# Optimization experiments

Hardware: AMD Instinct MI355X
Metric: run time of the kernel (lower is better)

The kernel has to match this reference:

```python
import jax, jax.numpy as jnp
import numpy as np

B = 4096
INPUT_DIM = 4096
N_BLOCKS = 8
BLOCK = INPUT_DIM // N_BLOCKS  # 512
N_EXPERTS = 6
H = 1024   # expert_hidden
H2 = H // 2


def setup_inputs() -> dict:
    key = jax.random.key(0)
    ks = jax.random.split(key, 16)
    s = 0.02  # init scale keeps tanh/softmax in sane range
    return {
        "x":   jax.random.normal(ks[0], (B, INPUT_DIM), jnp.float32),
        # routers: per-block stacked weights [8, ...]
        "Wr1": jax.random.normal(ks[1], (N_BLOCKS, BLOCK, 32), jnp.float32) * s,
        "br1": jax.random.normal(ks[2], (N_BLOCKS, 32), jnp.float32) * s,
        "Wr2": jax.random.normal(ks[3], (N_BLOCKS, 32, N_EXPERTS), jnp.float32) * s,
        "br2": jax.random.normal(ks[4], (N_BLOCKS, N_EXPERTS), jnp.float32) * s,
        # experts: stacked [6, ...], shared across all 8 blocks
        "We1": jax.random.normal(ks[5], (N_EXPERTS, BLOCK, H), jnp.float32) * s,
        "be1": jax.random.normal(ks[6], (N_EXPERTS, H), jnp.float32) * s,
        "We2": jax.random.normal(ks[7], (N_EXPERTS, H, H2), jnp.float32) * s,
        "be2": jax.random.normal(ks[8], (N_EXPERTS, H2), jnp.float32) * s,
        "We3": jax.random.normal(ks[9], (N_EXPERTS, H2, 3), jnp.float32) * s,
        "be3": jax.random.normal(ks[10], (N_EXPERTS, 3), jnp.float32) * s,
        # aggregator
        "Wa1": jax.random.normal(ks[11], (3, 16), jnp.float32) * s,
        "ba1": jax.random.normal(ks[12], (16,), jnp.float32) * s,
        "Wa2": jax.random.normal(ks[13], (16, 3), jnp.float32) * s,
        "ba2": jax.random.normal(ks[14], (3,), jnp.float32) * s,
    }


def reference(x, Wr1, br1, Wr2, br2, We1, be1, We2, be2, We3, be3,
              Wa1, ba1, Wa2, ba2):
    b = x.shape[0]
    blocks = x.reshape(b, N_BLOCKS, BLOCK)                       # [b,s,d]
    # routers (one per block s)
    r1 = jax.nn.relu(jnp.einsum('bsd,sdh->bsh', blocks, Wr1) + br1)
    routing = jax.nn.softmax(
        jnp.einsum('bsh,she->bse', r1, Wr2) + br2, axis=-1)      # [b,s,E]
    # experts applied to every block (grouped GEMMs)
    h1 = jnp.tanh(jnp.einsum('bsd,edh->bseh', blocks, We1) + be1)        # [b,s,E,H]
    h2 = jnp.tanh(jnp.einsum('bseh,ehk->bsek', h1, We2) + be2)           # [b,s,E,H2]
    eo = jnp.einsum('bsek,eko->bseo', h2, We3) + be3                     # [b,s,E,3]
    weighted = jnp.einsum('bse,bseo->bso', routing, eo)                  # [b,s,3]
    final = weighted.mean(axis=1)                                        # mean over 8 blocks
    a1 = jax.nn.relu(final @ Wa1 + ba1)
    return a1 @ Wa2 + ba2                                                # [b,3]
```

## Files before the change

kernel.cpp:

```cpp
#include <hip/hip_runtime.h>
#include <cstdint>
#include <cstddef>

typedef __bf16 bf16;
typedef __bf16 bf16x4 __attribute__((ext_vector_type(4)));
typedef __bf16 bf16x8 __attribute__((ext_vector_type(8)));
typedef float  f32x4  __attribute__((ext_vector_type(4)));
typedef long long i64v;

#define NROWS   32768
#define DBLK    512
#define H1N     1024
#define H2N     512
#define NEXP    6
#define NBATCH  4096
#define HALL    (NEXP * H1N)
#define W2SCALE 32.0f
#define W2INV   0.03125f

__device__ __forceinline__ void gld16(const void* g, void* l) {
    __builtin_amdgcn_global_load_lds(
        (const __attribute__((address_space(1))) void*)g,
        (__attribute__((address_space(3))) void*)l, 16, 0, 0);
}

__device__ __forceinline__ float fast_tanh(float x) {
    float e = __expf(2.0f * x);
    return 1.0f - __fdividef(2.0f, e + 1.0f);
}

__device__ __forceinline__ float hsum16(float v) {
    v += __shfl_xor(v, 1);
    v += __shfl_xor(v, 2);
    v += __shfl_xor(v, 4);
    v += __shfl_xor(v, 8);
    return v;
}

__device__ __forceinline__ int swz(int row, int g) {
    return row * 64 + ((g ^ (row & 7)) * 8);
}
__device__ __forceinline__ int swz8(int row, int g) {
    return row * 64 + ((g ^ ((row >> 1) & 3)) << 4);
}


__global__ void cvt_bf16_kernel(const float* __restrict__ in,
                                bf16* __restrict__ out, int n4) {
    int i = blockIdx.x * blockDim.x + threadIdx.x;
    if (i >= n4) return;
    float4 v = ((const float4*)in)[i];
    bf16x4 o;
    o.x = (bf16)v.x; o.y = (bf16)v.y; o.z = (bf16)v.z; o.w = (bf16)v.w;
    ((bf16x4*)out)[i] = o;
}

__global__ __launch_bounds__(256) void transpose_cvt(
    const float* __restrict__ in, bf16* __restrict__ out, int K, int N) {
    __shared__ bf16 tile[64][66];
    int e  = blockIdx.z;
    int n0 = blockIdx.x * 64;
    int k0 = blockIdx.y * 64;
    int c  = threadIdx.x & 63;
    int rb = threadIdx.x >> 6;
    const float* src = in + (size_t)e * K * N;
    bf16* dst = out + (size_t)e * N * K;
#pragma unroll
    for (int it = 0; it < 16; ++it) {
        int k = k0 + rb + it * 4;
        int n = n0 + c;
        if (k < K && n < N) tile[rb + it * 4][c] = (bf16)src[(size_t)k * N + n];
    }
    __syncthreads();
#pragma unroll
    for (int it = 0; it < 16; ++it) {
        int n = n0 + rb + it * 4;
        int k = k0 + c;
        if (n < N && k < K) dst[(size_t)n * K + k] = tile[c][rb + it * 4];
    }
}

__global__ __launch_bounds__(256) void transpose_cvt_fp8(
    const float* __restrict__ in, uint8_t* __restrict__ out, int K, int N,
    float scale) {
    __shared__ float tile[64][65];
    int e  = blockIdx.z;
    int n0 = blockIdx.x * 64;
    int k0 = blockIdx.y * 64;
    int c  = threadIdx.x & 63;
    int rb = threadIdx.x >> 6;
    const float* src = in + (size_t)e * K * N;
    uint8_t* dst = out + (size_t)e * N * K;
#pragma unroll
    for (int it = 0; it < 16; ++it) {
        int k = k0 + rb + it * 4;
        int n = n0 + c;
        if (k < K && n < N) tile[rb + it * 4][c] = src[(size_t)k * N + n];
    }
    __syncthreads();
#pragma unroll
    for (int it = 0; it < 16; ++it) {
        int n = n0 + rb + it * 4;
        int k = k0 + c;
        if (n < N && k < K) {
            float v = tile[c][rb + it * 4] * scale;
            int p = __builtin_amdgcn_cvt_pk_fp8_f32(v, v, 0, false);
            dst[(size_t)n * K + k] = (uint8_t)(p & 0xff);
        }
    }
}

__global__ void zero_f32_kernel(float* __restrict__ p, int n) {
    int i = blockIdx.x * blockDim.x + threadIdx.x;
    if (i < n) p[i] = 0.0f;
}


__global__ __launch_bounds__(256, 2) void router_kernel(
    const bf16* __restrict__ xbf,
    const bf16* __restrict__ Wr1t,
    const float* __restrict__ br1,
    const float* __restrict__ Wr2,
    const float* __restrict__ br2,
    float* __restrict__ routing) {
    __shared__ __align__(16) bf16 sA[128 * 64];
    __shared__ __align__(16) bf16 sB[32 * 64];
    const int tid = threadIdx.x;
    const int w = tid >> 6, l = tid & 63;
    const int s  = blockIdx.y;
    const int b0 = blockIdx.x * 128;
    const int wm = w * 32;
    const int srow = l >> 3, schk = (l & 7) * 8;
    const int fr = l & 15, fq = l >> 4;
    const bf16* Ab = xbf + (size_t)s * 512;
    const bf16* Bb = Wr1t + (size_t)s * (32 * 512);

    f32x4 acc[2][2];
#pragma unroll
    for (int i = 0; i < 2; ++i)
#pragma unroll
        for (int j = 0; j < 2; ++j) acc[i][j] = (f32x4){0.f, 0.f, 0.f, 0.f};

    for (int k0 = 0; k0 < 512; k0 += 64) {
        __syncthreads();
#pragma unroll
        for (int jj = 0; jj < 4; ++jj) {
            int row = w * 32 + jj * 8;
            gld16(Ab + (size_t)(b0 + row + srow) * 4096 + k0 + schk, sA + row * 64);
        }
        gld16(Bb + (size_t)(w * 8 + srow) * 512 + k0 + schk, sB + w * 8 * 64);
        __syncthreads();
#pragma unroll
        for (int ks = 0; ks < 2; ++ks) {
            bf16x8 af[2], bfr[2];
#pragma unroll
            for (int i = 0; i < 2; ++i)
                af[i] = *(const bf16x8*)&sA[(wm + i * 16 + fr) * 64 + ks * 32 + fq * 8];
#pragma unroll
            for (int j = 0; j < 2; ++j)
                bfr[j] = *(const bf16x8*)&sB[(j * 16 + fr) * 64 + ks * 32 + fq * 8];
#pragma unroll
            for (int i = 0; i < 2; ++i)
#pragma unroll
                for (int j = 0; j < 2; ++j)
                    acc[i][j] = __builtin_amdgcn_mfma_f32_16x16x32_bf16(
                        af[i], bfr[j], acc[i][j], 0, 0, 0);
        }
    }

    float b1v[2], w2v[2][6], br2v[6];
#pragma unroll
    for (int j = 0; j < 2; ++j) {
        int col = j * 16 + fr;
        b1v[j] = br1[s * 32 + col];
#pragma unroll
        for (int e2 = 0; e2 < 6; ++e2) w2v[j][e2] = Wr2[(s * 32 + col) * 6 + e2];
    }
#pragma unroll
    for (int e2 = 0; e2 < 6; ++e2) br2v[e2] = br2[s * 6 + e2];

#pragma unroll
    for (int i = 0; i < 2; ++i) {
#pragma unroll
        for (int r = 0; r < 4; ++r) {
            float lg[6] = {0.f, 0.f, 0.f, 0.f, 0.f, 0.f};
#pragma unroll
            for (int j = 0; j < 2; ++j) {
                float t = fmaxf(acc[i][j][r] + b1v[j], 0.f);
#pragma unroll
                for (int e2 = 0; e2 < 6; ++e2) lg[e2] += t * w2v[j][e2];
            }
#pragma unroll
            for (int e2 = 0; e2 < 6; ++e2) lg[e2] = hsum16(lg[e2]) + br2v[e2];
            float mx = lg[0];
#pragma unroll
            for (int e2 = 1; e2 < 6; ++e2) mx = fmaxf(mx, lg[e2]);
            float p[6], sum = 0.f;
#pragma unroll
            for (int e2 = 0; e2 < 6; ++e2) { p[e2] = __expf(lg[e2] - mx); sum += p[e2]; }
            float inv = __fdividef(1.f, sum);
            if (fr == 0) {
                int brow = b0 + wm + i * 16 + fq * 4 + r;
                float* dst = routing + ((size_t)brow * 8 + s) * 6;
#pragma unroll
                for (int e2 = 0; e2 < 6; ++e2) dst[e2] = p[e2] * inv;
            }
        }
    }
}

__global__ __launch_bounds__(256, 4) void gemm1_kernel(
    const bf16* __restrict__ A,
    const bf16* __restrict__ B,
    const float* __restrict__ bias,
    uint8_t* __restrict__ h1,
    int ldh) {
    __shared__ __align__(16) bf16 sA[128 * 64];
    __shared__ __align__(16) bf16 sB[128 * 64];
    const int tid = threadIdx.x;
    const int w = tid >> 6, l = tid & 63;
    const int n0 = blockIdx.x * 128;
    const int m0 = blockIdx.y * 128;
    const int wm = (w & 1) * 64, wn = (w >> 1) * 64;
    const int srow = l >> 3;
    const int gcol = ((l & 7) ^ srow) * 8;
    const int fr = l & 15, fq = l >> 4;

    f32x4 acc[4][4];
#pragma unroll
    for (int i = 0; i < 4; ++i)
#pragma unroll
        for (int j = 0; j < 4; ++j) acc[i][j] = (f32x4){0.f, 0.f, 0.f, 0.f};

    for (int k0 = 0; k0 < DBLK; k0 += 64) {
        __syncthreads();
#pragma unroll
        for (int jj = 0; jj < 4; ++jj) {
            int row = w * 32 + jj * 8;
            gld16(A + (size_t)(m0 + row + srow) * DBLK + k0 + gcol, sA + row * 64);
            gld16(B + (size_t)(n0 + row + srow) * DBLK + k0 + gcol, sB + row * 64);
        }
        __syncthreads();
#pragma unroll
        for (int ks = 0; ks < 2; ++ks) {
            bf16x8 af[4], bfr[4];
#pragma unroll
            for (int i = 0; i < 4; ++i)
                af[i] = *(const bf16x8*)&sA[swz(wm + i * 16 + fr, ks * 4 + fq)];
#pragma unroll
            for (int j = 0; j < 4; ++j)
                bfr[j] = *(const bf16x8*)&sB[swz(wn + j * 16 + fr, ks * 4 + fq)];
#pragma unroll
            for (int i = 0; i < 4; ++i)
#pragma unroll
                for (int j = 0; j < 4; ++j)
                    acc[i][j] = __builtin_amdgcn_mfma_f32_16x16x32_bf16(
                        af[i], bfr[j], acc[i][j], 0, 0, 0);
        }
    }

#pragma unroll
    for (int i = 0; i < 4; ++i) {
        int colb = m0 + wm + i * 16 + fq * 4;
        float4 bb = *(const float4*)&bias[colb];
#pragma unroll
        for (int j = 0; j < 4; ++j) {
            int xrow = n0 + wn + j * 16 + fr;
            float t0 = fast_tanh(acc[i][j][0] + bb.x);
            float t1 = fast_tanh(acc[i][j][1] + bb.y);
            float t2 = fast_tanh(acc[i][j][2] + bb.z);
            float t3 = fast_tanh(acc[i][j][3] + bb.w);
            int p = 0;
            p = __builtin_amdgcn_cvt_pk_fp8_f32(t0, t1, p, false);
            p = __builtin_amdgcn_cvt_pk_fp8_f32(t2, t3, p, true);
            *(uint32_t*)&h1[(size_t)xrow * ldh + colb] = (uint32_t)p;
        }
    }
}

__global__ __launch_bounds__(256, 4) void gemm2_kernel(
    const uint8_t* __restrict__ h1,
    const uint8_t* __restrict__ W2f8t,
    const float* __restrict__ be2,
    const float* __restrict__ We3,
    float* __restrict__ eo,
    int ldh) {
    __shared__ __align__(16) uint8_t sA[128 * 64];
    __shared__ __align__(16) uint8_t sB[128 * 64];
    __shared__ float w3s[128 * 3];
    __shared__ float b2s[128];
    const int tid = threadIdx.x;
    const int w = tid >> 6, l = tid & 63;
    const int e  = blockIdx.z;
    const int n0 = blockIdx.x * 128;
    const int m0 = blockIdx.y * 128;
    const int wm = (w & 1) * 64, wn = (w >> 1) * 64;
    const int srow4 = l >> 2;
    const int g4 = (((l & 3) ^ ((l >> 3) & 3)) << 4);
    const int fr = l & 15, fq = l >> 4;
    const uint8_t* Ae = W2f8t + (size_t)e * (H2N * H1N);
    const uint8_t* Be = h1 + (size_t)e * H1N;

    if (tid < 128) {
        int c = m0 + tid;
        b2s[tid] = be2[e * H2N + c];
        w3s[tid * 3 + 0] = We3[((size_t)e * H2N + c) * 3 + 0];
        w3s[tid * 3 + 1] = We3[((size_t)e * H2N + c) * 3 + 1];
        w3s[tid * 3 + 2] = We3[((size_t)e * H2N + c) * 3 + 2];
    }

    f32x4 acc[4][4];
#pragma unroll
    for (int i = 0; i < 4; ++i)
#pragma unroll
        for (int j = 0; j < 4; ++j) acc[i][j] = (f32x4){0.f, 0.f, 0.f, 0.f};

    for (int k0 = 0; k0 < H1N; k0 += 64) {
        __syncthreads();
#pragma unroll
        for (int jj = 0; jj < 2; ++jj) {
            int row = w * 32 + jj * 16 + srow4;
            gld16(Ae + (size_t)(m0 + row) * H1N + k0 + g4, sA + (w * 32 + jj * 16) * 64);
            gld16(Be + (size_t)(n0 + row) * ldh + k0 + g4, sB + (w * 32 + jj * 16) * 64);
        }
        __syncthreads();
#pragma unroll
        for (int ks = 0; ks < 2; ++ks) {
            i64v af[4], bfr[4];
#pragma unroll
            for (int i = 0; i < 4; ++i) {
                int row = wm + i * 16 + fr;
                af[i] = *(const i64v*)&sA[swz8(row, ks * 2 + (fq >> 1)) + ((fq & 1) << 3)];
            }
#pragma unroll
            for (int j = 0; j < 4; ++j) {
                int row = wn + j * 16 + fr;
                bfr[j] = *(const i64v*)&sB[swz8(row, ks * 2 + (fq >> 1)) + ((fq & 1) << 3)];
            }
#pragma unroll
            for (int i = 0; i < 4; ++i)
#pragma unroll
                for (int j = 0; j < 4; ++j)
                    acc[i][j] = __builtin_amdgcn_mfma_f32_16x16x32_fp8_fp8(
                        af[i], bfr[j], acc[i][j], 0, 0, 0);
        }
    }

    float p[4][3];
#pragma unroll
    for (int j = 0; j < 4; ++j) { p[j][0] = 0.f; p[j][1] = 0.f; p[j][2] = 0.f; }
#pragma unroll
    for (int i = 0; i < 4; ++i) {
        int cl = wm + i * 16 + fq * 4;
        float4 bb = *(const float4*)&b2s[cl];
        float4 wa = *(const float4*)&w3s[cl * 3 + 0];
        float4 wb = *(const float4*)&w3s[cl * 3 + 4];
        float4 wc = *(const float4*)&w3s[cl * 3 + 8];
        float bias4[4] = {bb.x, bb.y, bb.z, bb.w};
        float w30[4] = {wa.x, wa.w, wb.z, wc.y};
        float w31[4] = {wa.y, wb.x, wb.w, wc.z};
        float w32[4] = {wa.z, wb.y, wc.x, wc.w};
#pragma unroll
        for (int j = 0; j < 4; ++j) {
#pragma unroll
            for (int r = 0; r < 4; ++r) {
                float t = fast_tanh(acc[i][j][r] * W2INV + bias4[r]);
                p[j][0] += t * w30[r];
                p[j][1] += t * w31[r];
                p[j][2] += t * w32[r];
            }
        }
    }
#pragma unroll
    for (int j = 0; j < 4; ++j) {
        float v0 = p[j][0], v1 = p[j][1], v2 = p[j][2];
        v0 += __shfl_xor(v0, 16); v0 += __shfl_xor(v0, 32);
        v1 += __shfl_xor(v1, 16); v1 += __shfl_xor(v1, 32);
        v2 += __shfl_xor(v2, 16); v2 += __shfl_xor(v2, 32);
        if (fq == 0) {
            int xrow = n0 + wn + j * 16 + fr;
            float* dst = eo + ((size_t)e * NROWS + xrow) * 3;
            atomicAdd(dst + 0, v0);
            atomicAdd(dst + 1, v1);
            atomicAdd(dst + 2, v2);
        }
    }
}

__global__ void final_kernel(
    const float* __restrict__ routing, const float* __restrict__ eo,
    const float* __restrict__ be3, const float* __restrict__ Wa1,
    const float* __restrict__ ba1, const float* __restrict__ Wa2,
    const float* __restrict__ ba2, float* __restrict__ out) {
    int b = blockIdx.x * blockDim.x + threadIdx.x;
    if (b >= NBATCH) return;
    float f0 = 0.f, f1 = 0.f, f2 = 0.f;
    for (int s = 0; s < 8; ++s) {
        int r = b * 8 + s;
        const float* rt = routing + (size_t)r * 6;
#pragma unroll
        for (int e = 0; e < 6; ++e) {
            float wgt = rt[e];
            const float* eop = eo + ((size_t)e * NROWS + r) * 3;
            f0 += wgt * (eop[0] + be3[e * 3 + 0]);
            f1 += wgt * (eop[1] + be3[e * 3 + 1]);
            f2 += wgt * (eop[2] + be3[e * 3 + 2]);
        }
    }
    f0 *= 0.125f; f1 *= 0.125f; f2 *= 0.125f;
    float o0 = ba2[0], o1 = ba2[1], o2 = ba2[2];
#pragma unroll
    for (int h = 0; h < 16; ++h) {
        float a = f0 * Wa1[h] + f1 * Wa1[16 + h] + f2 * Wa1[32 + h] + ba1[h];
        a = fmaxf(a, 0.f);
        o0 += a * Wa2[h * 3 + 0];
        o1 += a * Wa2[h * 3 + 1];
        o2 += a * Wa2[h * 3 + 2];
    }
    out[b * 3 + 0] = o0;
    out[b * 3 + 1] = o1;
    out[b * 3 + 2] = o2;
}


extern "C" void kernel_launch(void* const* d_in, const int* in_sizes, int n_in,
                              void* d_out, int out_size, void* d_ws, size_t ws_size,
                              hipStream_t stream) {
    const float* x   = (const float*)d_in[0];
    const float* Wr1 = (const float*)d_in[1];
    const float* br1 = (const float*)d_in[2];
    const float* Wr2 = (const float*)d_in[3];
    const float* br2 = (const float*)d_in[4];
    const float* We1 = (const float*)d_in[5];
    const float* be1 = (const float*)d_in[6];
    const float* We2 = (const float*)d_in[7];
    const float* be2 = (const float*)d_in[8];
    const float* We3 = (const float*)d_in[9];
    const float* be3 = (const float*)d_in[10];
    const float* Wa1 = (const float*)d_in[11];
    const float* ba1 = (const float*)d_in[12];
    const float* Wa2 = (const float*)d_in[13];
    const float* ba2 = (const float*)d_in[14];
    float* out = (float*)d_out;

    char* ws = (char*)d_ws;
    const size_t off_xbf  = 0;
    const size_t off_w1t  = off_xbf  + (size_t)33554432;
    const size_t off_w2t  = off_w1t  + (size_t)6291456;
    const size_t off_wr1t = off_w2t  + (size_t)6291456;
    const size_t off_rout = off_wr1t + (size_t)262144;
    const size_t off_eo   = off_rout + (size_t)786432;
    const size_t off_h1   = off_eo   + (size_t)2359296;

    if (off_h1 + (size_t)NROWS * HALL > ws_size) return;

    bf16*    xbf     = (bf16*)(ws + off_xbf);
    bf16*    W1t     = (bf16*)(ws + off_w1t);
    uint8_t* W2f8t   = (uint8_t*)(ws + off_w2t);
    bf16*    Wr1t    = (bf16*)(ws + off_wr1t);
    float*   routing = (float*)(ws + off_rout);
    float*   eo      = (float*)(ws + off_eo);
    uint8_t* h1      = (uint8_t*)(ws + off_h1);

    cvt_bf16_kernel<<<16384, 256, 0, stream>>>(x, xbf, 4194304);
    transpose_cvt<<<dim3(16, 8, 6), 256, 0, stream>>>(We1, W1t, 512, 1024);
    transpose_cvt_fp8<<<dim3(8, 16, 6), 256, 0, stream>>>(We2, W2f8t, 1024, 512, W2SCALE);
    transpose_cvt<<<dim3(1, 8, 8), 256, 0, stream>>>(Wr1, Wr1t, 512, 32);
    zero_f32_kernel<<<2304, 256, 0, stream>>>(eo, 589824);

    router_kernel<<<dim3(32, 8), 256, 0, stream>>>(xbf, Wr1t, br1, Wr2, br2, routing);

    gemm1_kernel<<<dim3(NROWS / 128, HALL / 128), 256, 0, stream>>>(
        W1t, xbf, be1, h1, HALL);
    gemm2_kernel<<<dim3(NROWS / 128, H2N / 128, NEXP), 256, 0, stream>>>(
        h1, W2f8t, be2, We3, eo, HALL);

    final_kernel<<<16, 256, 0, stream>>>(routing, eo, be3, Wa1, ba1, Wa2, ba2, out);
}
```

Baseline: 675.6 us.

## Use 16x16x128 scaled FP8 MFMA in gemm2 with K=128 tiles

Switches the second expert GEMM from 16x16x32 fp8 MFMA to the gfx950 scaled 16x16x128 f8f6f4 MFMA with unit scales, doubling the K tile to 128 and rewriting the LDS swizzle and fragment loads to match. This cuts the number of MFMA issues and barrier round trips per K. In exchange it doubles LDS use per block and lowers the occupancy hint from 4 to 3. It also rewrites fast_tanh with exp2/rcp intrinsics and reorders the gemm1 epilogue so each thread's stores for a row are grouped together.

```diff
diff --git a/kernel.cpp b/kernel.cpp
--- a/kernel.cpp
+++ b/kernel.cpp
@@ -6,7 +6,8 @@
 typedef __bf16 bf16x4 __attribute__((ext_vector_type(4)));
 typedef __bf16 bf16x8 __attribute__((ext_vector_type(8)));
 typedef float  f32x4  __attribute__((ext_vector_type(4)));
-typedef long long i64v;
+typedef int    i32x4v __attribute__((ext_vector_type(4)));
+typedef int    i32x8v __attribute__((ext_vector_type(8)));
 
 #define NROWS   32768
 #define DBLK    512
@@ -25,8 +26,9 @@
 }
 
 __device__ __forceinline__ float fast_tanh(float x) {
-    float e = __expf(2.0f * x);
-    return 1.0f - __fdividef(2.0f, e + 1.0f);
+    float e = __builtin_amdgcn_exp2f(x * 2.8853900817779268f);
+    float r = __builtin_amdgcn_rcpf(e + 1.0f);
+    return __builtin_fmaf(-2.0f, r, 1.0f);
 }
 
 __device__ __forceinline__ float hsum16(float v) {
@@ -39,9 +41,6 @@
 
 __device__ __forceinline__ int swz(int row, int g) {
     return row * 64 + ((g ^ (row & 7)) * 8);
-}
-__device__ __forceinline__ int swz8(int row, int g) {
-    return row * 64 + ((g ^ ((row >> 1) & 3)) << 4);
 }
 
 
@@ -259,34 +258,37 @@
         }
     }
 
-#pragma unroll
-    for (int i = 0; i < 4; ++i) {
-        int colb = m0 + wm + i * 16 + fq * 4;
-        float4 bb = *(const float4*)&bias[colb];
-#pragma unroll
-        for (int j = 0; j < 4; ++j) {
-            int xrow = n0 + wn + j * 16 + fr;
-            float t0 = fast_tanh(acc[i][j][0] + bb.x);
-            float t1 = fast_tanh(acc[i][j][1] + bb.y);
-            float t2 = fast_tanh(acc[i][j][2] + bb.z);
-            float t3 = fast_tanh(acc[i][j][3] + bb.w);
+    float4 bb[4];
+#pragma unroll
+    for (int i = 0; i < 4; ++i)
+        bb[i] = *(const float4*)&bias[m0 + wm + i * 16 + fq * 4];
+#pragma unroll
+    for (int j = 0; j < 4; ++j) {
+        int xrow = n0 + wn + j * 16 + fr;
+        uint8_t* dst = &h1[(size_t)xrow * ldh + m0 + wm + fq * 4];
+#pragma unroll
+        for (int i = 0; i < 4; ++i) {
+            float t0 = fast_tanh(acc[i][j][0] + bb[i].x);
+            float t1 = fast_tanh(acc[i][j][1] + bb[i].y);
+            float t2 = fast_tanh(acc[i][j][2] + bb[i].z);
+            float t3 = fast_tanh(acc[i][j][3] + bb[i].w);
             int p = 0;
             p = __builtin_amdgcn_cvt_pk_fp8_f32(t0, t1, p, false);
             p = __builtin_amdgcn_cvt_pk_fp8_f32(t2, t3, p, true);
-            *(uint32_t*)&h1[(size_t)xrow * ldh + colb] = (uint32_t)p;
-        }
-    }
-}
-
-__global__ __launch_bounds__(256, 4) void gemm2_kernel(
+            *(uint32_t*)(dst + i * 16) = (uint32_t)p;
+        }
+    }
+}
+
+__global__ __launch_bounds__(256, 3) void gemm2_kernel(
     const uint8_t* __restrict__ h1,
     const uint8_t* __restrict__ W2f8t,
     const float* __restrict__ be2,
     const float* __restrict__ We3,
     float* __restrict__ eo,
     int ldh) {
-    __shared__ __align__(16) uint8_t sA[128 * 64];
-    __shared__ __align__(16) uint8_t sB[128 * 64];
+    __shared__ __align__(16) uint8_t sA[128 * 128];
+    __shared__ __align__(16) uint8_t sB[128 * 128];
     __shared__ float w3s[128 * 3];
     __shared__ float b2s[128];
     const int tid = threadIdx.x;
@@ -295,9 +297,9 @@
     const int n0 = blockIdx.x * 128;
     const int m0 = blockIdx.y * 128;
     const int wm = (w & 1) * 64, wn = (w >> 1) * 64;
-    const int srow4 = l >> 2;
-    const int g4 = (((l & 3) ^ ((l >> 3) & 3)) << 4);
     const int fr = l & 15, fq = l >> 4;
+    const int srow = l >> 3;
+    const int sgo = ((l & 7) ^ srow) * 16;
     const uint8_t* Ae = W2f8t + (size_t)e * (H2N * H1N);
     const uint8_t* Be = h1 + (size_t)e * H1N;
 
@@ -315,34 +317,38 @@
 #pragma unroll
         for (int j = 0; j < 4; ++j) acc[i][j] = (f32x4){0.f, 0.f, 0.f, 0.f};
 
-    for (int k0 = 0; k0 < H1N; k0 += 64) {
-        __syncthreads();
-#pragma unroll
-        for (int jj = 0; jj < 2; ++jj) {
-            int row = w * 32 + jj * 16 + srow4;
-            gld16(Ae + (size_t)(m0 + row) * H1N + k0 + g4, sA + (w * 32 + jj * 16) * 64);
-            gld16(Be + (size_t)(n0 + row) * ldh + k0 + g4, sB + (w * 32 + jj * 16) * 64);
-        }
-        __syncthreads();
-#pragma unroll
-        for (int ks = 0; ks < 2; ++ks) {
-            i64v af[4], bfr[4];
-#pragma unroll
-            for (int i = 0; i < 4; ++i) {
-                int row = wm + i * 16 + fr;
-                af[i] = *(const i64v*)&sA[swz8(row, ks * 2 + (fq >> 1)) + ((fq & 1) << 3)];
-            }
-#pragma unroll
-            for (int j = 0; j < 4; ++j) {
-                int row = wn + j * 16 + fr;
-                bfr[j] = *(const i64v*)&sB[swz8(row, ks * 2 + (fq >> 1)) + ((fq & 1) << 3)];
-            }
-#pragma unroll
-            for (int i = 0; i < 4; ++i)
-#pragma unroll
-                for (int j = 0; j < 4; ++j)
-                    acc[i][j] = __builtin_amdgcn_mfma_f32_16x16x32_fp8_fp8(
-                        af[i], bfr[j], acc[i][j], 0, 0, 0);
+    const int gA = ((2 * fq) ^ (fr & 7)) << 4;
+    const int gB = ((2 * fq + 1) ^ (fr & 7)) << 4;
+
+    for (int k0 = 0; k0 < H1N; k0 += 128) {
+        __syncthreads();
+#pragma unroll
+        for (int q = 0; q < 4; ++q) {
+            int row = w * 32 + q * 8 + srow;
+            gld16(Ae + (size_t)(m0 + row) * H1N + k0 + sgo,
+                  sA + (w * 32 + q * 8) * 128);
+            gld16(Be + (size_t)(n0 + row) * ldh + k0 + sgo,
+                  sB + (w * 32 + q * 8) * 128);
+        }
+        __syncthreads();
+        i32x8v bfr[4];
+#pragma unroll
+        for (int j = 0; j < 4; ++j) {
+            int row = wn + j * 16 + fr;
+            i32x4v bl = *(const i32x4v*)&sB[row * 128 + gA];
+            i32x4v bh = *(const i32x4v*)&sB[row * 128 + gB];
+            bfr[j] = __builtin_shufflevector(bl, bh, 0, 1, 2, 3, 4, 5, 6, 7);
+        }
+#pragma unroll
+        for (int i = 0; i < 4; ++i) {
+            int row = wm + i * 16 + fr;
+            i32x4v al = *(const i32x4v*)&sA[row * 128 + gA];
+            i32x4v ah = *(const i32x4v*)&sA[row * 128 + gB];
+            i32x8v a = __builtin_shufflevector(al, ah, 0, 1, 2, 3, 4, 5, 6, 7);
+#pragma unroll
+            for (int j = 0; j < 4; ++j)
+                acc[i][j] = __builtin_amdgcn_mfma_scale_f32_16x16x128_f8f6f4(
+                    a, bfr[j], acc[i][j], 0, 0, 0, 127, 0, 127);
         }
     }
 
```

Measured after the change: 700.6 us. 1.04x slower.
